# Optimization experiments

Measured on AMD Instinct MI355X. Metric: run time of the kernel, lower is better.

The kernel has to match this reference:

```python
import jax, jax.numpy as jnp
import numpy as np

N_NODES = 100000


def _gin_layer(x, edge_index, Wa, ba, Wb, bb):
    # GINConv, eps=0: h_i = MLP(x_i + sum_{j->i} x_j)
    src, dst = edge_index[0], edge_index[1]
    agg = jax.ops.segment_sum(x[src], dst, num_segments=N_NODES)  # [N, d]
    h = x + agg
    h = jax.nn.relu(h @ Wa + ba) @ Wb + bb
    return h


def setup_inputs() -> dict:
    key = jax.random.key(0)
    ks = jax.random.split(key, 8)
    d_in, d_h, E = 128, 128, 1600000
    scale_in = 1.0 / np.sqrt(d_in)
    scale_h = 1.0 / np.sqrt(d_h)
    return {
        "x": jax.random.normal(ks[0], (N_NODES, d_in), dtype=jnp.float32),
        "edge_index": jax.random.randint(ks[1], (2, E), 0, N_NODES, dtype=jnp.int64),
        "batch": jnp.zeros((N_NODES,), dtype=jnp.int64),
        "W1a": jax.random.normal(ks[2], (d_in, d_h), dtype=jnp.float32) * scale_in,
        "b1a": jnp.zeros((d_h,), dtype=jnp.float32),
        "W1b": jax.random.normal(ks[3], (d_h, d_h), dtype=jnp.float32) * scale_h,
        "b1b": jnp.zeros((d_h,), dtype=jnp.float32),
        "W2a": jax.random.normal(ks[4], (d_h, d_h), dtype=jnp.float32) * scale_h,
        "b2a": jnp.zeros((d_h,), dtype=jnp.float32),
        "W2b": jax.random.normal(ks[5], (d_h, d_h), dtype=jnp.float32) * scale_h,
        "b2b": jnp.zeros((d_h,), dtype=jnp.float32),
    }


def reference(x, edge_index, batch, W1a, b1a, W1b, b1b, W2a, b2a, W2b, b2b):
    h = jax.nn.relu(_gin_layer(x, edge_index, W1a, b1a, W1b, b1b))
    h = jax.nn.relu(_gin_layer(h, edge_index, W2a, b2a, W2b, b2b))
    return h
```

## Files before the change

### kernel.cpp

```cpp
#include <hip/hip_runtime.h>
#include <hip/hip_bf16.h>

#define D 128
#define EPB 4096
#define CAP 6144

typedef float f32x4 __attribute__((ext_vector_type(4)));
typedef float f32x2 __attribute__((ext_vector_type(2)));
typedef short short8 __attribute__((ext_vector_type(8)));


__device__ __forceinline__ unsigned bf16_rtn_bits(float x) {
    unsigned u = __float_as_uint(x);
    return (u + 0x7fffu + ((u >> 16) & 1u)) >> 16;
}

__device__ __forceinline__ f32x2 pkadd(f32x2 a, f32x2 b) {
    f32x2 d;
    asm("v_pk_add_f32 %0, %1, %2" : "=v"(d) : "v"(a), "v"(b));
    return d;
}

__device__ __forceinline__ void addbf8p(f32x2* acc, uint4 v) {
    f32x2 p0 = {__uint_as_float(v.x << 16), __uint_as_float(v.x & 0xffff0000u)};
    f32x2 p1 = {__uint_as_float(v.y << 16), __uint_as_float(v.y & 0xffff0000u)};
    f32x2 p2 = {__uint_as_float(v.z << 16), __uint_as_float(v.z & 0xffff0000u)};
    f32x2 p3 = {__uint_as_float(v.w << 16), __uint_as_float(v.w & 0xffff0000u)};
    acc[0] = pkadd(acc[0], p0);
    acc[1] = pkadd(acc[1], p1);
    acc[2] = pkadd(acc[2], p2);
    acc[3] = pkadd(acc[3], p3);
}


__global__ __launch_bounds__(256) void k_xtobf(const float4* __restrict__ X, uint4* __restrict__ O,
                                               int n8, int* __restrict__ gz, int nzero) {
    int i = blockIdx.x * 256 + threadIdx.x;
    if (i < nzero) gz[i] = 0;
    if (i >= n8) return;
    float4 a = X[2 * i], b = X[2 * i + 1];
    uint4 o;
    o.x = bf16_rtn_bits(a.x) | (bf16_rtn_bits(a.y) << 16);
    o.y = bf16_rtn_bits(a.z) | (bf16_rtn_bits(a.w) << 16);
    o.z = bf16_rtn_bits(b.x) | (bf16_rtn_bits(b.y) << 16);
    o.w = bf16_rtn_bits(b.z) | (bf16_rtn_bits(b.w) << 16);
    O[i] = o;
}

__global__ void k_wsplit4(const float* __restrict__ W1a, const float* __restrict__ W1b,
                          const float* __restrict__ W2a, const float* __restrict__ W2b,
                          unsigned short* __restrict__ Wt) {
    int m = blockIdx.x >> 6;
    int i = (blockIdx.x & 63) * 256 + threadIdx.x;
    const float* W = (m == 0) ? W1a : (m == 1) ? W1b : (m == 2) ? W2a : W2b;
    int k = i >> 7, n = i & 127;
    Wt[m * 16384 + n * 128 + k] = (unsigned short)bf16_rtn_bits(W[i]);
}


__global__ __launch_bounds__(256) void k_bin(const int* __restrict__ src,
                                             const int* __restrict__ dst, int E,
                                             int* __restrict__ gCursor,
                                             unsigned* __restrict__ binned) {
    __shared__ int cnt[512];
    __shared__ int offs[512];
    __shared__ int c2[512];
    __shared__ int gOff[512];
    __shared__ int s[256];
    __shared__ unsigned staged[EPB];
    __shared__ unsigned short bo[EPB];
    int t = threadIdx.x;
    cnt[t] = 0; cnt[t + 256] = 0;
    c2[t] = 0; c2[t + 256] = 0;
    __syncthreads();

    unsigned pk[EPB / 256];
    int bk[EPB / 256];
    int e0 = blockIdx.x * EPB;
#pragma unroll
    for (int i = 0; i < EPB / 256; ++i) {
        int e = e0 + i * 256 + t;
        int b = -1; unsigned p = 0;
        if (e < E) {
            int dv = dst[e], sv = src[e];
            b = dv >> 8;
            p = ((unsigned)sv << 8) | (unsigned)(dv & 255);
            atomicAdd(&cnt[b], 1);
        }
        pk[i] = p; bk[i] = b;
    }
    __syncthreads();
    int v0 = cnt[2 * t], v1 = cnt[2 * t + 1];
    int ps = v0 + v1;
    s[t] = ps;
    __syncthreads();
    for (int off = 1; off < 256; off <<= 1) {
        int tv = (t >= off) ? s[t - off] : 0;
        __syncthreads();
        s[t] += tv;
        __syncthreads();
    }
    int ex = s[t] - ps;
    offs[2 * t] = ex;
    offs[2 * t + 1] = ex + v0;
    if (cnt[2 * t])     gOff[2 * t]     = atomicAdd(&gCursor[2 * t], cnt[2 * t]);
    if (cnt[2 * t + 1]) gOff[2 * t + 1] = atomicAdd(&gCursor[2 * t + 1], cnt[2 * t + 1]);
    __syncthreads();
#pragma unroll
    for (int i = 0; i < EPB / 256; ++i) {
        int b = bk[i];
        if (b >= 0) {
            int p = offs[b] + atomicAdd(&c2[b], 1);
            staged[p] = pk[i];
            bo[p] = (unsigned short)b;
        }
    }
    __syncthreads();
    int total = s[255];
    for (int p = t; p < total; p += 256) {
        int b = bo[p];
        binned[(size_t)b * CAP + gOff[b] + (p - offs[b])] = staged[p];
    }
}

__global__ __launch_bounds__(256) void k_csr(const unsigned* __restrict__ binned,
                                             const int* __restrict__ bucketCnt,
                                             int* __restrict__ alloc,
                                             int2* __restrict__ rowse,
                                             int* __restrict__ colA,
                                             int Nn) {
    __shared__ int hist[256], loc[256], cur[256], s[256];
    __shared__ int baseSh;
    int t = threadIdx.x, b = blockIdx.x;
    int n = bucketCnt[b];
    const unsigned* bp = binned + (size_t)b * CAP;
    hist[t] = 0; cur[t] = 0;
    __syncthreads();
    for (int i = t; i < n; i += 256) atomicAdd(&hist[bp[i] & 255u], 1);
    __syncthreads();
    int v = hist[t];
    s[t] = v;
    __syncthreads();
    for (int off = 1; off < 256; off <<= 1) {
        int tv = (t >= off) ? s[t - off] : 0;
        __syncthreads();
        s[t] += tv;
        __syncthreads();
    }
    loc[t] = s[t] - v;
    if (t == 255) baseSh = atomicAdd(alloc, s[255]);
    __syncthreads();
    int base = baseSh;
    int node = b * 256 + t;
    if (node < Nn) rowse[node] = make_int2(base + loc[t], base + loc[t] + v);
    for (int i = t; i < n; i += 256) {
        unsigned w = bp[i];
        int dl = (int)(w & 255u);
        int p = atomicAdd(&cur[dl], 1);
        colA[base + loc[dl] + p] = (int)(w >> 8);
    }
}


__global__ __launch_bounds__(256) void agg_bf16(const unsigned short* __restrict__ X,
                                                const int2* __restrict__ rowse,
                                                const int* __restrict__ colA,
                                                unsigned short* __restrict__ H, int nnodes) {
    int node = blockIdx.x * 4 + (threadIdx.x >> 6);
    if (node >= nnodes) return;
    int lane = threadIdx.x & 63;
    int qt = lane >> 4, slot = lane & 15;
    const uint4* x4 = (const uint4*)X;
    size_t base = (size_t)node * 16 + slot;

    int2 se = rowse[node];
    int e = se.x, end = se.y;

    f32x2 acc[4] = {{0.f, 0.f}, {0.f, 0.f}, {0.f, 0.f}, {0.f, 0.f}};
    f32x2 acc2[4] = {{0.f, 0.f}, {0.f, 0.f}, {0.f, 0.f}, {0.f, 0.f}};
    if (qt == 0) addbf8p(acc, x4[base]);

    for (; e + 16 <= end; e += 16) {
        int s0 = colA[e + qt];
        int s1 = colA[e + 4 + qt];
        int s2 = colA[e + 8 + qt];
        int s3 = colA[e + 12 + qt];
        uint4 v0 = x4[(size_t)s0 * 16 + slot];
        uint4 v1 = x4[(size_t)s1 * 16 + slot];
        uint4 v2 = x4[(size_t)s2 * 16 + slot];
        uint4 v3 = x4[(size_t)s3 * 16 + slot];
        addbf8p(acc, v0);
        addbf8p(acc2, v1);
        addbf8p(acc, v2);
        addbf8p(acc2, v3);
    }
    if (e + 8 <= end) {
        int s0 = colA[e + qt];
        int s1 = colA[e + 4 + qt];
        uint4 v0 = x4[(size_t)s0 * 16 + slot];
        uint4 v1 = x4[(size_t)s1 * 16 + slot];
        addbf8p(acc, v0);
        addbf8p(acc2, v1);
        e += 8;
    }
    for (; e < end; e += 4) {
        int idx = e + qt;
        if (idx < end) {
            int s = colA[idx];
            addbf8p(acc, x4[(size_t)s * 16 + slot]);
        }
    }
    float a8[8];
#pragma unroll
    for (int j = 0; j < 4; ++j) {
        f32x2 t = pkadd(acc[j], acc2[j]);
        a8[2 * j] = t[0];
        a8[2 * j + 1] = t[1];
    }
#pragma unroll
    for (int j = 0; j < 8; ++j) {
        a8[j] += __shfl_xor(a8[j], 16);
        a8[j] += __shfl_xor(a8[j], 32);
    }
    if (qt == 0) {
        uint4 o;
        o.x = bf16_rtn_bits(a8[0]) | (bf16_rtn_bits(a8[1]) << 16);
        o.y = bf16_rtn_bits(a8[2]) | (bf16_rtn_bits(a8[3]) << 16);
        o.z = bf16_rtn_bits(a8[4]) | (bf16_rtn_bits(a8[5]) << 16);
        o.w = bf16_rtn_bits(a8[6]) | (bf16_rtn_bits(a8[7]) << 16);
        ((uint4*)H)[base] = o;
    }
}


template <bool OUT_BF16>
__global__ __launch_bounds__(256) void mlp_mfma(const unsigned short* __restrict__ Hb,
                                                const unsigned short* __restrict__ WaT,
                                                const float* __restrict__ ba,
                                                const unsigned short* __restrict__ WbT,
                                                const float* __restrict__ bb,
                                                void* __restrict__ OutP, int nrows) {
    __shared__ unsigned short sh[64 * 128];
    const int tid = threadIdx.x;
    const int rows0 = blockIdx.x * 64;
    const int nvalid = min(64, nrows - rows0);

    const int wv = tid >> 6, l = tid & 63, q = l >> 4, cl = l & 15;

    short8 B1[2][4], B2[2][4];
#pragma unroll
    for (int cf = 0; cf < 2; ++cf) {
        const unsigned short* wa = WaT + (size_t)(wv * 32 + cf * 16 + cl) * 128 + q * 8;
        const unsigned short* wb = WbT + (size_t)(wv * 32 + cf * 16 + cl) * 128 + q * 8;
#pragma unroll
        for (int kk = 0; kk < 4; ++kk) {
            B1[cf][kk] = *(const short8*)(wa + kk * 32);
            B2[cf][kk] = *(const short8*)(wb + kk * 32);
        }
    }

    {
        const uint4* src = (const uint4*)(Hb + (size_t)rows0 * 128);
#pragma unroll
        for (int it = 0; it < 4; ++it) {
            int idx = it * 256 + tid;
            int row = idx >> 4, s16 = idx & 15;
            uint4 v = {0u, 0u, 0u, 0u};
            if (row < nvalid) v = src[idx];
            int byteoff = (row << 8) + ((s16 << 4) ^ ((row & 7) << 4));
            *(uint4*)((char*)sh + byteoff) = v;
        }
    }
    __syncthreads();

    f32x4 acc[4][2];
#pragma unroll
    for (int cf = 0; cf < 2; ++cf) {
        float bv = ba[wv * 32 + cf * 16 + cl];
        f32x4 a = {bv, bv, bv, bv};
#pragma unroll
        for (int m = 0; m < 4; ++m) acc[m][cf] = a;
    }
#pragma unroll
    for (int kk = 0; kk < 4; ++kk) {
        short8 a[4];
#pragma unroll
        for (int m = 0; m < 4; ++m) {
            int row = m * 16 + cl;
            int byteoff = (row << 8) + ((kk * 64 + q * 16) ^ ((row & 7) << 4));
            a[m] = *(const short8*)((const char*)sh + byteoff);
        }
#pragma unroll
        for (int m = 0; m < 4; ++m)
#pragma unroll
            for (int cf = 0; cf < 2; ++cf)
                acc[m][cf] = __builtin_amdgcn_mfma_f32_16x16x32_bf16(a[m], B1[cf][kk], acc[m][cf], 0, 0, 0);
    }
    __syncthreads();

#pragma unroll
    for (int m = 0; m < 4; ++m)
#pragma unroll
        for (int cf = 0; cf < 2; ++cf)
#pragma unroll
            for (int r = 0; r < 4; ++r) {
                int row = m * 16 + q * 4 + r;
                int col = wv * 32 + cf * 16 + cl;
                int byteoff = (row << 8) + ((col * 2) ^ ((row & 7) << 4));
                *(unsigned short*)((char*)sh + byteoff) =
                    (unsigned short)bf16_rtn_bits(fmaxf(acc[m][cf][r], 0.f));
            }
    __syncthreads();

#pragma unroll
    for (int cf = 0; cf < 2; ++cf) {
        float bv = bb[wv * 32 + cf * 16 + cl];
        f32x4 a = {bv, bv, bv, bv};
#pragma unroll
        for (int m = 0; m < 4; ++m) acc[m][cf] = a;
    }
#pragma unroll
    for (int kk = 0; kk < 4; ++kk) {
        short8 a[4];
#pragma unroll
        for (int m = 0; m < 4; ++m) {
            int row = m * 16 + cl;
            int byteoff = (row << 8) + ((kk * 64 + q * 16) ^ ((row & 7) << 4));
            a[m] = *(const short8*)((const char*)sh + byteoff);
        }
#pragma unroll
        for (int m = 0; m < 4; ++m)
#pragma unroll
            for (int cf = 0; cf < 2; ++cf)
                acc[m][cf] = __builtin_amdgcn_mfma_f32_16x16x32_bf16(a[m], B2[cf][kk], acc[m][cf], 0, 0, 0);
    }

#pragma unroll
    for (int m = 0; m < 4; ++m)
#pragma unroll
        for (int cf = 0; cf < 2; ++cf)
#pragma unroll
            for (int r = 0; r < 4; ++r) {
                int row = m * 16 + q * 4 + r;
                if (row < nvalid) {
                    float v = fmaxf(acc[m][cf][r], 0.f);
                    size_t gi = ((size_t)rows0 + row) * 128 + wv * 32 + cf * 16 + cl;
                    if (OUT_BF16)
                        ((unsigned short*)OutP)[gi] = (unsigned short)bf16_rtn_bits(v);
                    else
                        ((float*)OutP)[gi] = v;
                }
            }
}


extern "C" void kernel_launch(void* const* d_in, const int* in_sizes, int n_in,
                              void* d_out, int out_size, void* d_ws, size_t ws_size,
                              hipStream_t stream) {
    const float* x  = (const float*)d_in[0];
    const int*   ei = (const int*)d_in[1];
    const float* W1a = (const float*)d_in[3];
    const float* b1a = (const float*)d_in[4];
    const float* W1b = (const float*)d_in[5];
    const float* b1b = (const float*)d_in[6];
    const float* W2a = (const float*)d_in[7];
    const float* b2a = (const float*)d_in[8];
    const float* W2b = (const float*)d_in[9];
    const float* b2b = (const float*)d_in[10];
    float* out = (float*)d_out;

    const int Nn = in_sizes[0] / D;
    const int E  = in_sizes[1] / 2;
    const int* srcIdx = ei;
    const int* dstIdx = ei + E;
    const int NB = (Nn + 255) >> 8;

    char* w = (char*)d_ws;
    size_t off = 0;
    int2* rowse = (int2*)(w + off);    off += (size_t)Nn * 8;
    off = (off + 255) & ~(size_t)255;
    int* gCursor = (int*)(w + off);    off += (size_t)(NB + 1) * 4;
    int* alloc = gCursor + NB;
    off = (off + 255) & ~(size_t)255;
    int* colA = (int*)(w + off);       off += (size_t)E * 4;
    off = (off + 255) & ~(size_t)255;
    unsigned short* wsp = (unsigned short*)(w + off); off += (size_t)4 * 16384 * 2;
    off = (off + 255) & ~(size_t)255;
    unsigned short* bufA = (unsigned short*)(w + off); off += (size_t)Nn * 128 * 2;
    off = (off + 255) & ~(size_t)255;
    unsigned short* bufB = (unsigned short*)(w + off);
    unsigned* binned = (unsigned*)bufB;

    unsigned short* W1aT = wsp + 0 * 16384;
    unsigned short* W1bT = wsp + 1 * 16384;
    unsigned short* W2aT = wsp + 2 * 16384;
    unsigned short* W2bT = wsp + 3 * 16384;

    const int gBin = (E + EPB - 1) / EPB;

    k_xtobf<<<(Nn * 16 + 255) / 256, 256, 0, stream>>>((const float4*)x, (uint4*)bufA,
                                                       Nn * 16, gCursor, NB + 1);
    k_wsplit4<<<256, 256, 0, stream>>>(W1a, W1b, W2a, W2b, wsp);

    k_bin<<<gBin, 256, 0, stream>>>(srcIdx, dstIdx, E, gCursor, binned);
    k_csr<<<NB, 256, 0, stream>>>(binned, gCursor, alloc, rowse, colA, Nn);

    const int gAgg = (Nn + 3) / 4;
    const int gMlp = (Nn + 63) / 64;

    agg_bf16<<<gAgg, 256, 0, stream>>>(bufA, rowse, colA, bufB, Nn);
    mlp_mfma<true><<<gMlp, 256, 0, stream>>>(bufB, W1aT, b1a, W1bT, b1b, (void*)bufA, Nn);
    agg_bf16<<<gAgg, 256, 0, stream>>>(bufA, rowse, colA, bufB, Nn);
    mlp_mfma<false><<<gMlp, 256, 0, stream>>>(bufB, W2aT, b2a, W2bT, b2b, (void*)out, Nn);
}
```

Before: 234.0 us.

## Split neighbor aggregation into two feature-half passes for cache locality

The gather-sum aggregation is split into two launches, each covering half of the 128 bf16 features (128 bytes per row), with 8 lanes per row and 8 edges in flight per wavefront. Each pass touches a 12.8MB working set of half-rows, which is meant to fit better in L2/MALL and raise hit rates on random neighbor gathers. The cost is reading colA and rowse twice, an extra launch, and 64-byte partial-sector accesses per gathered row.

```diff
diff --git a/kernel.cpp b/kernel.cpp
--- a/kernel.cpp
+++ b/kernel.cpp
@@ -162,52 +162,54 @@
 }
 
 
-__global__ __launch_bounds__(256) void agg_bf16(const unsigned short* __restrict__ X,
+__global__ __launch_bounds__(256) void agg_half(const unsigned short* __restrict__ X,
                                                 const int2* __restrict__ rowse,
                                                 const int* __restrict__ colA,
-                                                unsigned short* __restrict__ H, int nnodes) {
+                                                unsigned short* __restrict__ H,
+                                                int nnodes, int half) {
     int node = blockIdx.x * 4 + (threadIdx.x >> 6);
     if (node >= nnodes) return;
     int lane = threadIdx.x & 63;
-    int qt = lane >> 4, slot = lane & 15;
+    int oct = lane >> 3, slot = lane & 7;
     const uint4* x4 = (const uint4*)X;
-    size_t base = (size_t)node * 16 + slot;
+    size_t rbase = (size_t)node * 16 + half * 8 + slot;
+    const size_t hoff = half * 8 + slot;
 
     int2 se = rowse[node];
     int e = se.x, end = se.y;
 
     f32x2 acc[4] = {{0.f, 0.f}, {0.f, 0.f}, {0.f, 0.f}, {0.f, 0.f}};
     f32x2 acc2[4] = {{0.f, 0.f}, {0.f, 0.f}, {0.f, 0.f}, {0.f, 0.f}};
-    if (qt == 0) addbf8p(acc, x4[base]);
-
-    for (; e + 16 <= end; e += 16) {
-        int s0 = colA[e + qt];
-        int s1 = colA[e + 4 + qt];
-        int s2 = colA[e + 8 + qt];
-        int s3 = colA[e + 12 + qt];
-        uint4 v0 = x4[(size_t)s0 * 16 + slot];
-        uint4 v1 = x4[(size_t)s1 * 16 + slot];
-        uint4 v2 = x4[(size_t)s2 * 16 + slot];
-        uint4 v3 = x4[(size_t)s3 * 16 + slot];
+    if (oct == 0) addbf8p(acc, x4[rbase]);
+
+    for (; e + 32 <= end; e += 32) {
+        int i0 = colA[e + oct];
+        int i1 = colA[e + 8 + oct];
+        int i2 = colA[e + 16 + oct];
+        int i3 = colA[e + 24 + oct];
+        uint4 v0 = x4[(size_t)i0 * 16 + hoff];
+        uint4 v1 = x4[(size_t)i1 * 16 + hoff];
+        uint4 v2 = x4[(size_t)i2 * 16 + hoff];
+        uint4 v3 = x4[(size_t)i3 * 16 + hoff];
         addbf8p(acc, v0);
         addbf8p(acc2, v1);
         addbf8p(acc, v2);
         addbf8p(acc2, v3);
     }
-    if (e + 8 <= end) {
-        int s0 = colA[e + qt];
-        int s1 = colA[e + 4 + qt];
-        uint4 v0 = x4[(size_t)s0 * 16 + slot];
-        uint4 v1 = x4[(size_t)s1 * 16 + slot];
+    if (e + 16 <= end) {
+        int i0 = colA[e + oct];
+        int i1 = colA[e + 8 + oct];
+        uint4 v0 = x4[(size_t)i0 * 16 + hoff];
+        uint4 v1 = x4[(size_t)i1 * 16 + hoff];
         addbf8p(acc, v0);
         addbf8p(acc2, v1);
-        e += 8;
-    }
-    for (; e < end; e += 4) {
-        int idx = e + qt;
+        e += 16;
+    }
+    for (; e < end; e += 8) {
+        int idx = e + oct;
         if (idx < end) {
             int s = colA[idx];
-            addbf8p(acc, x4[(size_t)s * 16 + slot]);
+            addbf8p(acc, x4[(size_t)s * 16 + hoff]);
         }
     }
     float a8[8];
@@ -219,16 +221,17 @@
     }
 #pragma unroll
     for (int j = 0; j < 8; ++j) {
+        a8[j] += __shfl_xor(a8[j], 8);
         a8[j] += __shfl_xor(a8[j], 16);
         a8[j] += __shfl_xor(a8[j], 32);
     }
-    if (qt == 0) {
+    if (oct == 0) {
         uint4 o;
         o.x = bf16_rtn_bits(a8[0]) | (bf16_rtn_bits(a8[1]) << 16);
         o.y = bf16_rtn_bits(a8[2]) | (bf16_rtn_bits(a8[3]) << 16);
         o.z = bf16_rtn_bits(a8[4]) | (bf16_rtn_bits(a8[5]) << 16);
         o.w = bf16_rtn_bits(a8[6]) | (bf16_rtn_bits(a8[7]) << 16);
-        ((uint4*)H)[base] = o;
+        ((uint4*)H)[rbase] = o;
     }
 }
 
@@ -408,8 +411,10 @@
     const int gAgg = (Nn + 3) / 4;
     const int gMlp = (Nn + 63) / 64;
 
-    agg_bf16<<<gAgg, 256, 0, stream>>>(bufA, rowse, colA, bufB, Nn);
+    agg_half<<<gAgg, 256, 0, stream>>>(bufA, rowse, colA, bufB, Nn, 0);
+    agg_half<<<gAgg, 256, 0, stream>>>(bufA, rowse, colA, bufB, Nn, 1);
     mlp_mfma<true><<<gMlp, 256, 0, stream>>>(bufB, W1aT, b1a, W1bT, b1b, (void*)bufA, Nn);
-    agg_bf16<<<gAgg, 256, 0, stream>>>(bufA, rowse, colA, bufB, Nn);
+    agg_half<<<gAgg, 256, 0, stream>>>(bufA, rowse, colA, bufB, Nn, 0);
+    agg_half<<<gAgg, 256, 0, stream>>>(bufA, rowse, colA, bufB, Nn, 1);
     mlp_mfma<false><<<gMlp, 256, 0, stream>>>(bufB, W2aT, b2a, W2bT, b2b, (void*)out, Nn);
 }
```

Measured after the change: 273.4 us. 16.8% more time.
